# Kernel tuning notes

Hardware: AMD Instinct MI355X
Metric: run time of the kernel (lower is better)

## Reference

```python
import jax, jax.numpy as jnp
import numpy as np

B, N, C, S, G, COOR = 4, 8192, 64, 2048, 32, 3
C2 = 2 * C            # channels after SetAbstraction
EXP = 4
RADII = (0.2, 0.4, 0.4)


def _sqdist(src, dst):
    # (B,M,3),(B,N,3) -> (B,M,N) squared distances (same expansion as torch code)
    d = -2.0 * jnp.einsum('bmc,bnc->bmn', src, dst)
    d = d + jnp.sum(src ** 2, -1)[:, :, None]
    d = d + jnp.sum(dst ** 2, -1)[:, None, :]
    return d


def _gather(points, idx):
    # points (B,N,C), idx (B,...) -> (B,...,C)
    return jax.vmap(lambda p, i: p[i])(points, idx)


def _fps(xyz, npoint):
    # xyz (B,N,3) -> (B,npoint) farthest point sample indices (start at index 0)
    b, n, _ = xyz.shape

    def step(carry, _):
        distance, farthest = carry
        centroid = jnp.take_along_axis(xyz, farthest[:, None, None], axis=1)  # (B,1,3)
        d = jnp.sqrt(jnp.sum((xyz - centroid) ** 2, -1))
        distance = jnp.minimum(distance, d)
        nxt = jnp.argmax(distance, -1)
        return (distance, nxt), farthest

    init = (jnp.full((b, n), 1e10, xyz.dtype), jnp.zeros((b,), jnp.int32))
    _, idxs = jax.lax.scan(step, init, None, length=npoint)
    return jnp.transpose(idxs)  # (B,npoint)


def _query_hybrid(radius, nsample, xyz, new_xyz):
    d = _sqdist(new_xyz, xyz)                       # (B,S,N)
    neg_d, idx = jax.lax.top_k(-d, nsample)         # smallest distances
    mask = (-neg_d) > radius ** 2
    first = idx[:, :, :1]
    return jnp.where(mask, first, idx)              # (B,S,nsample)


def _group(coor, new_coor, fea, radius, nsample):
    # coor (B,N,3), new_coor (B,S,3), fea (B,N,C) -> (B,S,G,C+3)
    gi = _query_hybrid(radius, nsample, coor, new_coor)
    gc = (_gather(coor, gi) - new_coor[:, :, None, :]) / radius
    gf = _gather(fea, gi)
    return jnp.concatenate([gf, gc], axis=-1)


def _mlp_max(g, w):
    # g (B,S,G,Cin), w (Cout,Cin): 1x1 conv (no bias) + ReLU, then max over group
    h = jax.nn.relu(jnp.einsum('bsgc,dc->bsgd', g, w))
    return jnp.max(h, axis=2)  # (B,S,Cout)


def _inv_res_mlp(coor, fea, radius, nsample, w_la, w1, w2):
    # coor (B,S,3), fea (B,S,C2) channels-last
    identity = fea
    g = _group(coor, coor, fea, radius, nsample)
    fea = _mlp_max(g, w_la)                              # LocalAggregation
    fea = jax.nn.relu(jnp.einsum('bsc,dc->bsd', fea, w1))
    fea = jnp.einsum('bsc,dc->bsd', fea, w2)             # last ReLU dropped
    return jax.nn.relu(fea + identity)


def setup_inputs() -> dict:
    key = jax.random.key(0)
    ks = jax.random.split(key, 10)
    def w(k, o, i):
        return jax.random.normal(k, (o, i), jnp.float32) / np.sqrt(i)
    return {
        'points_coor': jax.random.uniform(ks[0], (B, 3, N), jnp.float32),
        'points_fea': jax.random.normal(ks[1], (B, C, N), jnp.float32),
        'w_sa':  w(ks[2], C2, C + COOR),
        'w_la1': w(ks[3], C2, C2 + COOR),
        'w1_1':  w(ks[4], C2 * EXP, C2),
        'w2_1':  w(ks[5], C2, C2 * EXP),
        'w_la2': w(ks[6], C2, C2 + COOR),
        'w1_2':  w(ks[7], C2 * EXP, C2),
        'w2_2':  w(ks[8], C2, C2 * EXP),
    }


def reference(points_coor, points_fea, w_sa, w_la1, w1_1, w2_1, w_la2, w1_2, w2_2):
    coor = jnp.transpose(points_coor, (0, 2, 1))  # (B,N,3)
    fea = jnp.transpose(points_fea, (0, 2, 1))    # (B,N,C)
    # SetAbstraction: S-G-P
    fps_idx = _fps(coor, S)
    new_coor = _gather(coor, fps_idx)             # (B,S,3)
    g = _group(coor, new_coor, fea, RADII[0], G)
    new_fea = _mlp_max(g, w_sa)                   # (B,S,2C)
    # InvResMLP blocks
    new_fea = _inv_res_mlp(new_coor, new_fea, RADII[1], G, w_la1, w1_1, w2_1)
    new_fea = _inv_res_mlp(new_coor, new_fea, RADII[2], G, w_la2, w1_2, w2_2)
    return (jnp.transpose(new_coor, (0, 2, 1)), jnp.transpose(new_fea, (0, 2, 1)))
```

## Files before the change

### kernel.cpp

```cpp
#include <hip/hip_runtime.h>
#include <hip/hip_bf16.h>

#define BB 4
#define NN 8192
#define CC 64
#define SS 2048
#define GG 32
#define C2V 128
#define HHV 512

typedef unsigned long long u64;
typedef unsigned int u32;

__global__ void k_transpose_fea(const float* __restrict__ in, float* __restrict__ out) {
  __shared__ float tile[32][33];
  const int b = blockIdx.z;
  const int n0 = blockIdx.x * 32, c0 = blockIdx.y * 32;
  const int tx = threadIdx.x, ty = threadIdx.y;
  const float* src = in + (size_t)b * CC * NN;
#pragma unroll
  for (int i = 0; i < 32; i += 8)
    tile[ty + i][tx] = src[(size_t)(c0 + ty + i) * NN + n0 + tx];
  __syncthreads();
  float* dst = out + (size_t)b * NN * CC;
#pragma unroll
  for (int i = 0; i < 32; i += 8)
    dst[(size_t)(n0 + ty + i) * CC + c0 + tx] = tile[tx][ty + i];
}

__global__ __launch_bounds__(1024, 4) void k_fps(const float* __restrict__ pc, int* __restrict__ fps_idx) {
#pragma clang fp contract(off)
  __shared__ float lx[NN], ly[NN], lz[NN];
  __shared__ int sIdx[SS];
  __shared__ u64 sK[2][16];
  const int b = blockIdx.x, tid = threadIdx.x;
  const int lane = tid & 63, wid = tid >> 6;
  const float* pb = pc + (size_t)b * 3 * NN;

  const float4* gx = (const float4*)pb;
  const float4* gy = (const float4*)(pb + NN);
  const float4* gz = (const float4*)(pb + 2 * NN);
  float4 vXa = gx[tid], vXb = gx[tid + 1024];
  float4 vYa = gy[tid], vYb = gy[tid + 1024];
  float4 vZa = gz[tid], vZb = gz[tid + 1024];
  {
    float4* sx = (float4*)lx; float4* sy = (float4*)ly; float4* sz = (float4*)lz;
    sx[tid] = vXa; sx[tid + 1024] = vXb;
    sy[tid] = vYa; sy[tid + 1024] = vYb;
    sz[tid] = vZa; sz[tid + 1024] = vZb;
  }
  float aXax, aXay, aXaz, aXaw, aXbx, aXby, aXbz, aXbw;
  float aYax, aYay, aYaz, aYaw, aYbx, aYby, aYbz, aYbw;
  float aZax, aZay, aZaz, aZaw, aZbx, aZby, aZbz, aZbw;
#define PARK(A, V) asm volatile("v_accvgpr_write_b32 %0, %1" : "=a"(A) : "v"(V));
  PARK(aXax, vXa.x) PARK(aXay, vXa.y) PARK(aXaz, vXa.z) PARK(aXaw, vXa.w)
  PARK(aXbx, vXb.x) PARK(aXby, vXb.y) PARK(aXbz, vXb.z) PARK(aXbw, vXb.w)
  PARK(aYax, vYa.x) PARK(aYay, vYa.y) PARK(aYaz, vYa.z) PARK(aYaw, vYa.w)
  PARK(aYbx, vYb.x) PARK(aYby, vYb.y) PARK(aYbz, vYb.z) PARK(aYbw, vYb.w)
  PARK(aZax, vZa.x) PARK(aZay, vZa.y) PARK(aZaz, vZa.z) PARK(aZaw, vZa.w)
  PARK(aZbx, vZb.x) PARK(aZby, vZb.y) PARK(aZbz, vZb.z) PARK(aZbw, vZb.w)
#undef PARK
  if (tid < 32) ((u64*)sK)[tid] = 0ull;
  if (tid == 0) sK[0][0] = ~0ull;
  __syncthreads();

  const u32 ibase = (u32)(wid * 256 + lane * 4);
  float4 D0 = make_float4(1e20f, 1e20f, 1e20f, 1e20f);
  float4 D1 = D0;

#define DPPK64(K, CTL) { \
      u32 lo = (u32)(K), hi = (u32)((K) >> 32); \
      u32 lo2 = (u32)__builtin_amdgcn_update_dpp(0, (int)lo, CTL, 0xf, 0xf, false); \
      u32 hi2 = (u32)__builtin_amdgcn_update_dpp(0, (int)hi, CTL, 0xf, 0xf, false); \
      u64 k2 = ((u64)hi2 << 32) | (u64)lo2; if (k2 > (K)) (K) = k2; }
#define RMAXF(V, CTL) { \
      float t_ = __int_as_float(__builtin_amdgcn_update_dpp(0, __float_as_int(V), CTL, 0xf, 0xf, false)); \
      (V) = fmaxf((V), t_); }
#define RMINU(V, CTL) { \
      u32 t_ = (u32)__builtin_amdgcn_update_dpp(0, (int)(V), CTL, 0xf, 0xf, false); \
      (V) = min((V), t_); }
#define FETCH(V, A) asm volatile("v_accvgpr_read_b32 %0, %1" : "=v"(V) : "a"(A));

  for (int k = 0; k < SS; ++k) {
    const int p = k & 1, pn = p ^ 1;
    u64 kk = sK[p][lane & 15];
    float xax, xay, xaz, xaw, xbx, xby, xbz, xbw;
    float yax, yay, yaz, yaw, ybx, yby, ybz, ybw;
    float zax, zay, zaz, zaw, zbx, zby, zbz, zbw;
    FETCH(xax, aXax) FETCH(xay, aXay) FETCH(xaz, aXaz) FETCH(xaw, aXaw)
    FETCH(xbx, aXbx) FETCH(xby, aXby) FETCH(xbz, aXbz) FETCH(xbw, aXbw)
    FETCH(yax, aYax) FETCH(yay, aYay) FETCH(yaz, aYaz) FETCH(yaw, aYaw)
    FETCH(ybx, aYbx) FETCH(yby, aYby) FETCH(ybz, aYbz) FETCH(ybw, aYbw)
    FETCH(zax, aZax) FETCH(zay, aZay) FETCH(zaz, aZaz) FETCH(zaw, aZaw)
    FETCH(zbx, aZbx) FETCH(zby, aZby) FETCH(zbz, aZbz) FETCH(zbw, aZbw)
    DPPK64(kk, 0x121) DPPK64(kk, 0x122) DPPK64(kk, 0x124) DPPK64(kk, 0x128)
    const u32 idx = 0xFFFFFFFFu - (u32)kk;
    if (tid == 0) sIdx[k] = (int)idx;
    const float cx = lx[idx], cy = ly[idx], cz = lz[idx];

#define UPDC(XX, YY, ZZ, DD) { \
      float dx_ = (XX) - cx, dy_ = (YY) - cy, dz_ = (ZZ) - cz; \
      float t0_ = dx_ * dx_, t1_ = dy_ * dy_, t2_ = dz_ * dz_; \
      float s_ = (t0_ + t1_) + t2_; \
      (DD) = fminf((DD), s_); }
    UPDC(xax, yax, zax, D0.x) UPDC(xay, yay, zay, D0.y)
    UPDC(xaz, yaz, zaz, D0.z) UPDC(xaw, yaw, zaw, D0.w)
    UPDC(xbx, ybx, zbx, D1.x) UPDC(xby, yby, zby, D1.y)
    UPDC(xbz, ybz, zbz, D1.z) UPDC(xbw, ybw, zbw, D1.w)
#undef UPDC

    float m2 = fmaxf(fmaxf(fmaxf(D0.x, D0.y), fmaxf(D0.z, D0.w)),
                     fmaxf(fmaxf(D1.x, D1.y), fmaxf(D1.z, D1.w)));
    RMAXF(m2, 0x121) RMAXF(m2, 0x122) RMAXF(m2, 0x124) RMAXF(m2, 0x128)
    m2 = fmaxf(m2, __shfl_xor(m2, 16, 64));
    m2 = fmaxf(m2, __shfl_xor(m2, 32, 64));

    float s = sqrtf(m2);
    u32 sbits = __float_as_uint(s);
    float spred = __uint_as_float(sbits - 1u);
    double M = ((double)spred + (double)s) * 0.5;
    double L = M * M;
    if (sbits & 1u) L = __longlong_as_double(__double_as_longlong(L) + 1ll);
    float Lf = (float)L;
    if ((double)Lf < L) Lf = __uint_as_float(__float_as_uint(Lf) + 1u);

    u32 enc = 0xFFFFFFFFu;
    {
      int off = -1;
      if (D1.w >= Lf) off = 4096 + 3;
      if (D1.z >= Lf) off = 4096 + 2;
      if (D1.y >= Lf) off = 4096 + 1;
      if (D1.x >= Lf) off = 4096 + 0;
      if (D0.w >= Lf) off = 3;
      if (D0.z >= Lf) off = 2;
      if (D0.y >= Lf) off = 1;
      if (D0.x >= Lf) off = 0;
      if (off >= 0) enc = ibase + (u32)off;
    }
    RMINU(enc, 0x121) RMINU(enc, 0x122) RMINU(enc, 0x124) RMINU(enc, 0x128)
    enc = min(enc, (u32)__shfl_xor((int)enc, 16, 64));
    enc = min(enc, (u32)__shfl_xor((int)enc, 32, 64));

    if (lane == 0)
      sK[pn][wid] = (((u64)sbits) << 32) | (u64)(0xFFFFFFFFu - enc);
    __syncthreads();
  }
#undef DPPK64
#undef RMAXF
#undef RMINU
#undef FETCH
  fps_idx[b * SS + tid] = sIdx[tid];
  fps_idx[b * SS + 1024 + tid] = sIdx[1024 + tid];
}

__global__ void k_gather(const float* __restrict__ pc, const int* __restrict__ fps_idx,
                         float* __restrict__ ncoor, float* __restrict__ out0) {
  int t = blockIdx.x * 256 + threadIdx.x;
  if (t >= BB * SS) return;
  int b = t / SS, s = t % SS;
  int id = fps_idx[t];
  const float* base = pc + (size_t)b * 3 * NN;
  float x = base[id], y = base[NN + id], z = base[2 * NN + id];
  ncoor[(size_t)t * 3] = x; ncoor[(size_t)t * 3 + 1] = y; ncoor[(size_t)t * 3 + 2] = z;
  size_t o = (size_t)b * 3 * SS + s;
  out0[o] = x; out0[o + SS] = y; out0[o + 2 * SS] = z;
}

__global__ __launch_bounds__(256) void k_knn(const float* __restrict__ candp,
                                             const float* __restrict__ newc,
                                             int mode, int ncand, float r2,
                                             int* __restrict__ gidx) {
  __shared__ float cd[2048];
  __shared__ int ci[2048];
  __shared__ int hist[64];
  __shared__ int cnt, oc, binT, mlow;
  const int q = blockIdx.x, tid = threadIdx.x;
  const int b = q / SS;
  if (tid == 0) { cnt = 0; oc = 0; }
  if (tid < 64) hist[tid] = 0;
  __syncthreads();
  const float qx = newc[(size_t)q * 3], qy = newc[(size_t)q * 3 + 1], qz = newc[(size_t)q * 3 + 2];
  float qn;
  {
#pragma clang fp contract(off)
    qn = (qx * qx + qy * qy) + qz * qz;
  }
  const float sc = 64.0f / r2;
  const float* base = (mode == 0) ? candp + (size_t)b * 3 * NN : candp + (size_t)b * SS * 3;
  for (int i = tid; i < ncand; i += 256) {
    float x, y, z;
    if (mode == 0) { x = base[i]; y = base[NN + i]; z = base[2 * NN + i]; }
    else { x = base[3 * i]; y = base[3 * i + 1]; z = base[3 * i + 2]; }
    float dot = fmaf(qz, z, fmaf(qy, y, qx * x));
    float d;
    {
#pragma clang fp contract(off)
      float pn = (x * x + y * y) + z * z;
      d = ((-2.0f * dot) + qn) + pn;
    }
    if (d <= r2) {
      int pp = atomicAdd(&cnt, 1);
      if (pp < 2048) { cd[pp] = d; ci[pp] = i; }
      float db = (d > 0.0f) ? d : 0.0f;
      atomicAdd(&hist[min(63, (int)(db * sc))], 1);
    }
  }
  __syncthreads();
  const int M = min(cnt, 2048);
  if (tid == 0) {
    if (M > 32) {
      int c = 0, t = 0;
      for (t = 0; t < 64; ++t) { if (c + hist[t] >= 32) break; c += hist[t]; }
      binT = t; mlow = c;
    } else binT = -1;
  }
  __syncthreads();
  int* out = gidx + (size_t)q * 32;
  if (binT < 0) {
    for (int j = tid; j < M; j += 256) out[atomicAdd(&oc, 1)] = ci[j];
    __syncthreads();
    if (tid == 0 && M < 32) {
      float bd = 1e30f; int bx = 0x7FFFFFFF;
      for (int j = 0; j < M; ++j)
        if (cd[j] < bd || (cd[j] == bd && ci[j] < bx)) { bd = cd[j]; bx = ci[j]; }
      for (int j = M; j < 32; ++j) out[j] = bx;
    }
  } else {
    const int bt = binT, m = mlow;
    for (int j = tid; j < M; j += 256) {
      float dbj = (cd[j] > 0.0f) ? cd[j] : 0.0f;
      int bin = min(63, (int)(dbj * sc));
      if (bin < bt) out[atomicAdd(&oc, 1)] = ci[j];
      else if (bin == bt) {
        int r = 0; const float dj = cd[j]; const int ij = ci[j];
        for (int kk = 0; kk < M; ++kk) {
          float dbk = (cd[kk] > 0.0f) ? cd[kk] : 0.0f;
          if (min(63, (int)(dbk * sc)) == bt &&
              (cd[kk] < dj || (cd[kk] == dj && ci[kk] < ij))) ++r;
        }
        if (m + r < 32) out[m + r] = ci[j];
      }
    }
  }
}

template <int FDIM>
__global__ __launch_bounds__(256) void k_group_mlp(
    const float* __restrict__ fea, const int* __restrict__ gidx,
    const float* __restrict__ newc, const float* __restrict__ candp,
    int mode, int ncand, float radius,
    const float* __restrict__ wp, float* __restrict__ outf) {
  constexpr int CP4 = FDIM + 4;
  constexpr int NC4 = CP4 / 4;
  __shared__ float4 g4[2][32][NC4];
  __shared__ int sidx[2][32];
  __shared__ float sq[2][3];
  __shared__ float pf[2][4][128];
  const int tid = threadIdx.x;
  const int rs = tid >> 7, tl = tid & 127;
  const int dt = tl & 31, et = tl >> 5;
  const int d0 = dt * 4, e0 = et * 8;
  const int row0 = blockIdx.x * 4;
  for (int rp = 0; rp < 4; rp += 2) {
    const int row = row0 + rp + rs;
    if (tl < 32) sidx[rs][tl] = gidx[(size_t)row * 32 + tl];
    if (tl < 3) sq[rs][tl] = newc[(size_t)row * 3 + tl];
    __syncthreads();
    const int bb2 = row / SS;
    const float* fb = fea + (size_t)bb2 * ncand * FDIM;
    const float* cb = (mode == 0) ? candp + (size_t)bb2 * 3 * NN
                                  : candp + (size_t)bb2 * SS * 3;
    float* gf = (float*)&g4[rs][0][0];
    for (int qq = tl; qq < 32 * CP4; qq += 128) {
      int e = qq / CP4, c = qq - e * CP4;
      int id = sidx[rs][e];
      float v;
      if (c < FDIM) v = fb[(size_t)id * FDIM + c];
      else if (c < FDIM + 3) {
        int comp = c - FDIM;
        float pcv = (mode == 0) ? cb[(size_t)comp * NN + id] : cb[(size_t)id * 3 + comp];
        v = (pcv - sq[rs][comp]) / radius;
      } else v = 0.0f;
      gf[qq] = v;
    }
    __syncthreads();
    float acc[4][8];
#pragma unroll
    for (int i = 0; i < 4; ++i)
#pragma unroll
      for (int j = 0; j < 8; ++j) acc[i][j] = 0.0f;
    const float4* w4 = (const float4*)wp;
    for (int c4 = 0; c4 < NC4; ++c4) {
      float4 wv[4], gv[8];
#pragma unroll
      for (int i = 0; i < 4; ++i) wv[i] = w4[(size_t)(d0 + i) * NC4 + c4];
#pragma unroll
      for (int j = 0; j < 8; ++j) gv[j] = g4[rs][e0 + j][c4];
#pragma unroll
      for (int i = 0; i < 4; ++i)
#pragma unroll
        for (int j = 0; j < 8; ++j) {
          acc[i][j] += wv[i].x * gv[j].x;
          acc[i][j] += wv[i].y * gv[j].y;
          acc[i][j] += wv[i].z * gv[j].z;
          acc[i][j] += wv[i].w * gv[j].w;
        }
    }
#pragma unroll
    for (int i = 0; i < 4; ++i) {
      float m = acc[i][0];
#pragma unroll
      for (int j = 1; j < 8; ++j) m = fmaxf(m, acc[i][j]);
      pf[rs][et][d0 + i] = m;
    }
    __syncthreads();
    {
      const int d = tid & 127, r2s = tid >> 7;
      const int rowW = row0 + rp + r2s;
      float m = fmaxf(fmaxf(pf[r2s][0][d], pf[r2s][1][d]),
                      fmaxf(pf[r2s][2][d], pf[r2s][3][d]));
      outf[(size_t)rowW * 128 + d] = fmaxf(m, 0.0f);
    }
    __syncthreads();
  }
}

template <bool RESID>
__global__ __launch_bounds__(256) void k_dense(
    const float* __restrict__ A, const float* __restrict__ W,
    const float* __restrict__ Id, float* __restrict__ Out,
    int K, int Ntot) {
  __shared__ float4 sa[64][17], sb[64][17];
  const int m0 = blockIdx.x * 64, n0 = blockIdx.y * 64;
  const int tid = threadIdx.x;
  const int mt = tid & 15, nt = tid >> 4;
  float acc[4][4];
#pragma unroll
  for (int i = 0; i < 4; ++i)
#pragma unroll
    for (int j = 0; j < 4; ++j) acc[i][j] = 0.0f;
  for (int kc = 0; kc < K; kc += 64) {
    for (int q2 = tid; q2 < 2048; q2 += 256) {
      int half = q2 >> 10, qq = q2 & 1023;
      int r = qq >> 4, c = qq & 15;
      const float* src = half ? (W + (size_t)(n0 + r) * K + kc + c * 4)
                              : (A + (size_t)(m0 + r) * K + kc + c * 4);
      float4 v = *(const float4*)src;
      if (half) sb[r][c] = v; else sa[r][c] = v;
    }
    __syncthreads();
#pragma unroll
    for (int c = 0; c < 16; ++c) {
      const int ks = (c + mt + nt) & 15;
      float4 av[4], bv[4];
#pragma unroll
      for (int i = 0; i < 4; ++i) av[i] = sa[mt * 4 + i][ks];
#pragma unroll
      for (int j = 0; j < 4; ++j) bv[j] = sb[nt * 4 + j][ks];
#pragma unroll
      for (int i = 0; i < 4; ++i)
#pragma unroll
        for (int j = 0; j < 4; ++j) {
          acc[i][j] += av[i].x * bv[j].x;
          acc[i][j] += av[i].y * bv[j].y;
          acc[i][j] += av[i].z * bv[j].z;
          acc[i][j] += av[i].w * bv[j].w;
        }
    }
    __syncthreads();
  }
#pragma unroll
  for (int i = 0; i < 4; ++i)
#pragma unroll
    for (int j = 0; j < 4; ++j) {
      size_t o = (size_t)(m0 + mt * 4 + i) * Ntot + n0 + nt * 4 + j;
      float v = acc[i][j];
      if (RESID) v += Id[o];
      Out[o] = fmaxf(v, 0.0f);
    }
}

__global__ void k_pad_w(const float* __restrict__ src, float* __restrict__ dst,
                        int rows, int cin, int cp4) {
  int t = blockIdx.x * 256 + threadIdx.x;
  if (t >= rows * cp4) return;
  int r = t / cp4, c = t - r * cp4;
  dst[t] = (c < cin) ? src[(size_t)r * cin + c] : 0.0f;
}

__global__ void k_out1_t(const float* __restrict__ in, float* __restrict__ out) {
  __shared__ float tile[32][33];
  const int b = blockIdx.z;
  const int s0 = blockIdx.x * 32, d0 = blockIdx.y * 32;
  const int tx = threadIdx.x, ty = threadIdx.y;
#pragma unroll
  for (int i = 0; i < 32; i += 8)
    tile[ty + i][tx] = in[(size_t)(b * SS + s0 + ty + i) * 128 + d0 + tx];
  __syncthreads();
#pragma unroll
  for (int i = 0; i < 32; i += 8)
    out[(size_t)(b * 128 + d0 + ty + i) * SS + s0 + tx] = tile[tx][ty + i];
}

extern "C" void kernel_launch(void* const* d_in, const int* in_sizes, int n_in,
                              void* d_out, int out_size, void* d_ws, size_t ws_size,
                              hipStream_t stream) {
  const float* pc    = (const float*)d_in[0];
  const float* pfea  = (const float*)d_in[1];
  const float* w_sa  = (const float*)d_in[2];
  const float* w_la1 = (const float*)d_in[3];
  const float* w1_1  = (const float*)d_in[4];
  const float* w2_1  = (const float*)d_in[5];
  const float* w_la2 = (const float*)d_in[6];
  const float* w1_2  = (const float*)d_in[7];
  const float* w2_2  = (const float*)d_in[8];
  float* out0 = (float*)d_out;
  float* out1 = out0 + (size_t)BB * 3 * SS;

  char* wsp = (char*)d_ws;
  size_t off = 0;
  auto alloc = [&](size_t bytes) -> void* {
    void* p = wsp + off;
    off = (off + bytes + 255) & ~(size_t)255;
    return p;
  };
  float* hbuf = (float*)alloc((size_t)BB * SS * HHV * 4);
  float* feaT = hbuf;
  int*   fpsi = (int*)alloc((size_t)BB * SS * 4);
  float* ncoor = (float*)alloc((size_t)BB * SS * 3 * 4);
  int*   gi = (int*)alloc((size_t)BB * SS * GG * 4);
  float* fa = (float*)alloc((size_t)BB * SS * C2V * 4);
  float* fb = (float*)alloc((size_t)BB * SS * C2V * 4);
  float* wsap = (float*)alloc(128 * 68 * 4);
  float* wla1p = (float*)alloc(128 * 132 * 4);
  float* wla2p = (float*)alloc(128 * 132 * 4);

  k_pad_w<<<dim3((128 * 68 + 255) / 256), dim3(256), 0, stream>>>(w_sa, wsap, 128, 67, 68);
  k_pad_w<<<dim3((128 * 132 + 255) / 256), dim3(256), 0, stream>>>(w_la1, wla1p, 128, 131, 132);
  k_pad_w<<<dim3((128 * 132 + 255) / 256), dim3(256), 0, stream>>>(w_la2, wla2p, 128, 131, 132);

  k_transpose_fea<<<dim3(NN / 32, CC / 32, BB), dim3(32, 8), 0, stream>>>(pfea, feaT);
  k_fps<<<dim3(BB), dim3(1024), 0, stream>>>(pc, fpsi);
  k_gather<<<dim3((BB * SS + 255) / 256), dim3(256), 0, stream>>>(pc, fpsi, ncoor, out0);

  k_knn<<<dim3(BB * SS), dim3(256), 0, stream>>>(pc, ncoor, 0, NN, 0.04f, gi);
  k_group_mlp<64><<<dim3(BB * SS / 4), dim3(256), 0, stream>>>(feaT, gi, ncoor, pc, 0, NN, 0.2f, wsap, fa);

  k_knn<<<dim3(BB * SS), dim3(256), 0, stream>>>(ncoor, ncoor, 1, SS, 0.16f, gi);

  k_group_mlp<128><<<dim3(BB * SS / 4), dim3(256), 0, stream>>>(fa, gi, ncoor, ncoor, 1, SS, 0.4f, wla1p, fb);
  k_dense<false><<<dim3(128, 8), dim3(256), 0, stream>>>(fb, w1_1, nullptr, hbuf, 128, 512);
  k_dense<true><<<dim3(128, 2), dim3(256), 0, stream>>>(hbuf, w2_1, fa, fb, 512, 128);

  k_group_mlp<128><<<dim3(BB * SS / 4), dim3(256), 0, stream>>>(fb, gi, ncoor, ncoor, 1, SS, 0.4f, wla2p, fa);
  k_dense<false><<<dim3(128, 8), dim3(256), 0, stream>>>(fa, w1_2, nullptr, hbuf, 128, 512);
  k_dense<true><<<dim3(128, 2), dim3(256), 0, stream>>>(hbuf, w2_2, fb, fa, 512, 128);

  k_out1_t<<<dim3(SS / 32, 128 / 32, BB), dim3(32, 8), 0, stream>>>(fa, out1);
}
```

Before: 4.112 ms.

## Process two queries per kNN block and chunk group MLP over neighbors

The kNN kernel now handles two query points per block, so each candidate coordinate load serves two distance computations and the grid is halved. Shared-memory buffers double to hold two candidate lists and histograms. The group-MLP kernel stages the 32 neighbors in two chunks of 16, which halves the gather tile in shared memory and the accumulator registers, with a running max kept across chunks. In exchange it adds extra barriers and reloads the weights for each chunk, while the larger kNN shared footprint may reduce occupancy.

```diff
diff --git a/kernel.cpp b/kernel.cpp
--- a/kernel.cpp
+++ b/kernel.cpp
@@ -170,20 +170,23 @@
                                              const float* __restrict__ newc,
                                              int mode, int ncand, float r2,
                                              int* __restrict__ gidx) {
-  __shared__ float cd[2048];
-  __shared__ int ci[2048];
-  __shared__ int hist[64];
-  __shared__ int cnt, oc, binT, mlow;
-  const int q = blockIdx.x, tid = threadIdx.x;
-  const int b = q / SS;
-  if (tid == 0) { cnt = 0; oc = 0; }
-  if (tid < 64) hist[tid] = 0;
-  __syncthreads();
-  const float qx = newc[(size_t)q * 3], qy = newc[(size_t)q * 3 + 1], qz = newc[(size_t)q * 3 + 2];
-  float qn;
+  __shared__ float cd[2][2048];
+  __shared__ int ci[2][2048];
+  __shared__ int hist[2][64];
+  __shared__ int cnt[2], oc[2], binT[2], mlow[2];
+  const int q0 = blockIdx.x * 2, tid = threadIdx.x;
+  const int b = q0 / SS;
+  if (tid == 0) { cnt[0] = 0; cnt[1] = 0; oc[0] = 0; oc[1] = 0; }
+  if (tid < 64) hist[0][tid] = 0;
+  else if (tid < 128) hist[1][tid - 64] = 0;
+  __syncthreads();
+  const float qx0 = newc[(size_t)q0 * 3], qy0 = newc[(size_t)q0 * 3 + 1], qz0 = newc[(size_t)q0 * 3 + 2];
+  const float qx1 = newc[(size_t)(q0 + 1) * 3], qy1 = newc[(size_t)(q0 + 1) * 3 + 1], qz1 = newc[(size_t)(q0 + 1) * 3 + 2];
+  float qn0, qn1;
   {
 #pragma clang fp contract(off)
-    qn = (qx * qx + qy * qy) + qz * qz;
+    qn0 = (qx0 * qx0 + qy0 * qy0) + qz0 * qz0;
+    qn1 = (qx1 * qx1 + qy1 * qy1) + qz1 * qz1;
   }
   const float sc = 64.0f / r2;
   const float* base = (mode == 0) ? candp + (size_t)b * 3 * NN : candp + (size_t)b * SS * 3;
@@ -191,56 +194,80 @@
     float x, y, z;
     if (mode == 0) { x = base[i]; y = base[NN + i]; z = base[2 * NN + i]; }
     else { x = base[3 * i]; y = base[3 * i + 1]; z = base[3 * i + 2]; }
-    float dot = fmaf(qz, z, fmaf(qy, y, qx * x));
-    float d;
     {
+      float dot = fmaf(qz0, z, fmaf(qy0, y, qx0 * x));
+      float d;
+      {
 #pragma clang fp contract(off)
-      float pn = (x * x + y * y) + z * z;
-      d = ((-2.0f * dot) + qn) + pn;
-    }
-    if (d <= r2) {
-      int pp = atomicAdd(&cnt, 1);
-      if (pp < 2048) { cd[pp] = d; ci[pp] = i; }
-      float db = (d > 0.0f) ? d : 0.0f;
-      atomicAdd(&hist[min(63, (int)(db * sc))], 1);
-    }
-  }
-  __syncthreads();
-  const int M = min(cnt, 2048);
+        float pn = (x * x + y * y) + z * z;
+        d = ((-2.0f * dot) + qn0) + pn;
+      }
+      if (d <= r2) {
+        int pp = atomicAdd(&cnt[0], 1);
+        if (pp < 2048) { cd[0][pp] = d; ci[0][pp] = i; }
+        float db = (d > 0.0f) ? d : 0.0f;
+        atomicAdd(&hist[0][min(63, (int)(db * sc))], 1);
+      }
+    }
+    {
+      float dot = fmaf(qz1, z, fmaf(qy1, y, qx1 * x));
+      float d;
+      {
+#pragma clang fp contract(off)
+        float pn = (x * x + y * y) + z * z;
+        d = ((-2.0f * dot) + qn1) + pn;
+      }
+      if (d <= r2) {
+        int pp = atomicAdd(&cnt[1], 1);
+        if (pp < 2048) { cd[1][pp] = d; ci[1][pp] = i; }
+        float db = (d > 0.0f) ? d : 0.0f;
+        atomicAdd(&hist[1][min(63, (int)(db * sc))], 1);
+      }
+    }
+  }
+  __syncthreads();
   if (tid == 0) {
-    if (M > 32) {
-      int c = 0, t = 0;
-      for (t = 0; t < 64; ++t) { if (c + hist[t] >= 32) break; c += hist[t]; }
-      binT = t; mlow = c;
-    } else binT = -1;
-  }
-  __syncthreads();
-  int* out = gidx + (size_t)q * 32;
-  if (binT < 0) {
-    for (int j = tid; j < M; j += 256) out[atomicAdd(&oc, 1)] = ci[j];
-    __syncthreads();
-    if (tid == 0 && M < 32) {
-      float bd = 1e30f; int bx = 0x7FFFFFFF;
-      for (int j = 0; j < M; ++j)
-        if (cd[j] < bd || (cd[j] == bd && ci[j] < bx)) { bd = cd[j]; bx = ci[j]; }
-      for (int j = M; j < 32; ++j) out[j] = bx;
-    }
-  } else {
-    const int bt = binT, m = mlow;
-    for (int j = tid; j < M; j += 256) {
-      float dbj = (cd[j] > 0.0f) ? cd[j] : 0.0f;
-      int bin = min(63, (int)(dbj * sc));
-      if (bin < bt) out[atomicAdd(&oc, 1)] = ci[j];
-      else if (bin == bt) {
-        int r = 0; const float dj = cd[j]; const int ij = ci[j];
-        for (int kk = 0; kk < M; ++kk) {
-          float dbk = (cd[kk] > 0.0f) ? cd[kk] : 0.0f;
-          if (min(63, (int)(dbk * sc)) == bt &&
-              (cd[kk] < dj || (cd[kk] == dj && ci[kk] < ij))) ++r;
+#pragma unroll
+    for (int jq = 0; jq < 2; ++jq) {
+      const int M = min(cnt[jq], 2048);
+      if (M > 32) {
+        int c = 0, t = 0;
+        for (t = 0; t < 64; ++t) { if (c + hist[jq][t] >= 32) break; c += hist[jq][t]; }
+        binT[jq] = t; mlow[jq] = c;
+      } else binT[jq] = -1;
+    }
+  }
+  __syncthreads();
+  for (int jq = 0; jq < 2; ++jq) {
+    const int M = min(cnt[jq], 2048);
+    int* out = gidx + (size_t)(q0 + jq) * 32;
+    if (binT[jq] < 0) {
+      for (int j = tid; j < M; j += 256) out[atomicAdd(&oc[jq], 1)] = ci[jq][j];
+      __syncthreads();
+      if (tid == 0 && M < 32) {
+        float bd = 1e30f; int bx = 0x7FFFFFFF;
+        for (int j = 0; j < M; ++j)
+          if (cd[jq][j] < bd || (cd[jq][j] == bd && ci[jq][j] < bx)) { bd = cd[jq][j]; bx = ci[jq][j]; }
+        for (int j = M; j < 32; ++j) out[j] = bx;
+      }
+    } else {
+      const int bt = binT[jq], m = mlow[jq];
+      for (int j = tid; j < M; j += 256) {
+        float dbj = (cd[jq][j] > 0.0f) ? cd[jq][j] : 0.0f;
+        int bin = min(63, (int)(dbj * sc));
+        if (bin < bt) out[atomicAdd(&oc[jq], 1)] = ci[jq][j];
+        else if (bin == bt) {
+          int r = 0; const float dj = cd[jq][j]; const int ij = ci[jq][j];
+          for (int kk = 0; kk < M; ++kk) {
+            float dbk = (cd[jq][kk] > 0.0f) ? cd[jq][kk] : 0.0f;
+            if (min(63, (int)(dbk * sc)) == bt &&
+                (cd[jq][kk] < dj || (cd[jq][kk] == dj && ci[jq][kk] < ij))) ++r;
+          }
+          if (m + r < 32) out[m + r] = ci[jq][j];
         }
-        if (m + r < 32) out[m + r] = ci[j];
-      }
-    }
+      }
+    }
+    __syncthreads();
   }
 }
 
@@ -252,14 +279,14 @@
     const float* __restrict__ wp, float* __restrict__ outf) {
   constexpr int CP4 = FDIM + 4;
   constexpr int NC4 = CP4 / 4;
-  __shared__ float4 g4[2][32][NC4];
+  __shared__ float4 g4[2][16][NC4];
   __shared__ int sidx[2][32];
   __shared__ float sq[2][3];
   __shared__ float pf[2][4][128];
   const int tid = threadIdx.x;
   const int rs = tid >> 7, tl = tid & 127;
   const int dt = tl & 31, et = tl >> 5;
-  const int d0 = dt * 4, e0 = et * 8;
+  const int d0 = dt * 4, e0 = et * 4;
   const int row0 = blockIdx.x * 4;
   for (int rp = 0; rp < 4; rp += 2) {
     const int row = row0 + rp + rs;
@@ -271,48 +298,53 @@
     const float* cb = (mode == 0) ? candp + (size_t)bb2 * 3 * NN
                                   : candp + (size_t)bb2 * SS * 3;
     float* gf = (float*)&g4[rs][0][0];
-    for (int qq = tl; qq < 32 * CP4; qq += 128) {
-      int e = qq / CP4, c = qq - e * CP4;
-      int id = sidx[rs][e];
-      float v;
-      if (c < FDIM) v = fb[(size_t)id * FDIM + c];
-      else if (c < FDIM + 3) {
-        int comp = c - FDIM;
-        float pcv = (mode == 0) ? cb[(size_t)comp * NN + id] : cb[(size_t)id * 3 + comp];
-        v = (pcv - sq[rs][comp]) / radius;
-      } else v = 0.0f;
-      gf[qq] = v;
-    }
-    __syncthreads();
-    float acc[4][8];
-#pragma unroll
-    for (int i = 0; i < 4; ++i)
-#pragma unroll
-      for (int j = 0; j < 8; ++j) acc[i][j] = 0.0f;
     const float4* w4 = (const float4*)wp;
-    for (int c4 = 0; c4 < NC4; ++c4) {
-      float4 wv[4], gv[8];
-#pragma unroll
-      for (int i = 0; i < 4; ++i) wv[i] = w4[(size_t)(d0 + i) * NC4 + c4];
-#pragma unroll
-      for (int j = 0; j < 8; ++j) gv[j] = g4[rs][e0 + j][c4];
+    float rmax[4];
+#pragma unroll
+    for (int i = 0; i < 4; ++i) rmax[i] = -1e30f;
+    for (int ec = 0; ec < 2; ++ec) {
+      for (int qq = tl; qq < 16 * CP4; qq += 128) {
+        int e = qq / CP4, c = qq - e * CP4;
+        int id = sidx[rs][ec * 16 + e];
+        float v;
+        if (c < FDIM) v = fb[(size_t)id * FDIM + c];
+        else if (c < FDIM + 3) {
+          int comp = c - FDIM;
+          float pcv = (mode == 0) ? cb[(size_t)comp * NN + id] : cb[(size_t)id * 3 + comp];
+          v = (pcv - sq[rs][comp]) / radius;
+        } else v = 0.0f;
+        gf[qq] = v;
+      }
+      __syncthreads();
+      float acc[4][4];
 #pragma unroll
       for (int i = 0; i < 4; ++i)
 #pragma unroll
-        for (int j = 0; j < 8; ++j) {
-          acc[i][j] += wv[i].x * gv[j].x;
-          acc[i][j] += wv[i].y * gv[j].y;
-          acc[i][j] += wv[i].z * gv[j].z;
-          acc[i][j] += wv[i].w * gv[j].w;
-        }
-    }
-#pragma unroll
-    for (int i = 0; i < 4; ++i) {
-      float m = acc[i][0];
-#pragma unroll
-      for (int j = 1; j < 8; ++j) m = fmaxf(m, acc[i][j]);
-      pf[rs][et][d0 + i] = m;
-    }
+        for (int j = 0; j < 4; ++j) acc[i][j] = 0.0f;
+      for (int c4 = 0; c4 < NC4; ++c4) {
+        float4 wv[4], gv[4];
+#pragma unroll
+        for (int i = 0; i < 4; ++i) wv[i] = w4[(size_t)(d0 + i) * NC4 + c4];
+#pragma unroll
+        for (int j = 0; j < 4; ++j) gv[j] = g4[rs][e0 + j][c4];
+#pragma unroll
+        for (int i = 0; i < 4; ++i)
+#pragma unroll
+          for (int j = 0; j < 4; ++j) {
+            acc[i][j] += wv[i].x * gv[j].x;
+            acc[i][j] += wv[i].y * gv[j].y;
+            acc[i][j] += wv[i].z * gv[j].z;
+            acc[i][j] += wv[i].w * gv[j].w;
+          }
+      }
+#pragma unroll
+      for (int i = 0; i < 4; ++i)
+#pragma unroll
+        for (int j = 0; j < 4; ++j) rmax[i] = fmaxf(rmax[i], acc[i][j]);
+      __syncthreads();
+    }
+#pragma unroll
+    for (int i = 0; i < 4; ++i) pf[rs][et][d0 + i] = rmax[i];
     __syncthreads();
     {
       const int d = tid & 127, r2s = tid >> 7;
@@ -443,10 +475,10 @@
   k_fps<<<dim3(BB), dim3(1024), 0, stream>>>(pc, fpsi);
   k_gather<<<dim3((BB * SS + 255) / 256), dim3(256), 0, stream>>>(pc, fpsi, ncoor, out0);
 
-  k_knn<<<dim3(BB * SS), dim3(256), 0, stream>>>(pc, ncoor, 0, NN, 0.04f, gi);
+  k_knn<<<dim3(BB * SS / 2), dim3(256), 0, stream>>>(pc, ncoor, 0, NN, 0.04f, gi);
   k_group_mlp<64><<<dim3(BB * SS / 4), dim3(256), 0, stream>>>(feaT, gi, ncoor, pc, 0, NN, 0.2f, wsap, fa);
 
-  k_knn<<<dim3(BB * SS), dim3(256), 0, stream>>>(ncoor, ncoor, 1, SS, 0.16f, gi);
+  k_knn<<<dim3(BB * SS / 2), dim3(256), 0, stream>>>(ncoor, ncoor, 1, SS, 0.16f, gi);
 
   k_group_mlp<128><<<dim3(BB * SS / 4), dim3(256), 0, stream>>>(fa, gi, ncoor, ncoor, 1, SS, 0.4f, wla1p, fb);
   k_dense<false><<<dim3(128, 8), dim3(256), 0, stream>>>(fb, w1_1, nullptr, hbuf, 128, 512);
```

Result: slower. 4.600 ms (median of 2 runs) (+11.9%).
